# Performance work log

Hardware: AMD Instinct MI355X
Metric: run time of the kernel (lower is better)

## Reference

```python
import jax, jax.numpy as jnp
import numpy as np

N = 100000

def gat_layer(x, src, dst, W, a_s, a_d, b, H, C, concat):
    # x: [N, F_in]; messages flow src -> dst, softmax grouped by dst (PyG GATConv)
    h = (x @ W).reshape(N, H, C)                       # [N,H,C]
    al_s = jnp.sum(h * a_s, axis=-1)                   # [N,H]
    al_d = jnp.sum(h * a_d, axis=-1)                   # [N,H]
    e = jax.nn.leaky_relu(al_s[src] + al_d[dst], 0.2)  # [E,H]
    m = jax.ops.segment_max(e, dst, num_segments=N)    # [N,H] per-dst max
    ex = jnp.exp(e - m[dst])
    s = jax.ops.segment_sum(ex, dst, num_segments=N)
    alpha = ex / (s[dst] + 1e-16)                      # [E,H]
    msg = h[src] * alpha[:, :, None]                   # [E,H,C]
    out = jax.ops.segment_sum(msg, dst, num_segments=N)  # [N,H,C]
    out = out.reshape(N, H * C) if concat else out.mean(axis=1)
    return out + b

def setup_inputs() -> dict:
    key = jax.random.key(0)
    ks = jax.random.split(key, 32)
    d = {}
    d['x'] = jax.random.normal(ks[0], (N, 128), dtype=jnp.float32)
    d['edge_index'] = jax.random.randint(ks[1], (2, 1600000), 0, N, dtype=jnp.int32)
    dims = [(128, 8, 8), (64, 8, 8), (64, 8, 8), (64, 8, 8), (64, 8, 40)]
    for i, (fin, H, C) in enumerate(dims, start=1):
        d[f'W{i}'] = jax.random.normal(ks[4 * i], (fin, H * C), dtype=jnp.float32) * 0.1
        d[f'as{i}'] = jax.random.normal(ks[4 * i + 1], (H, C), dtype=jnp.float32) * 0.1
        d[f'ad{i}'] = jax.random.normal(ks[4 * i + 2], (H, C), dtype=jnp.float32) * 0.1
        d[f'b{i}'] = jnp.zeros((H * C if i < 5 else C,), dtype=jnp.float32)
    return d

def reference(x, edge_index, W1, as1, ad1, b1, W2, as2, ad2, b2, W3, as3, ad3, b3, W4, as4, ad4, b4, W5, as5, ad5, b5):
    # add self-loops (PyG GATConv default add_self_loops=True)
    loop = jnp.arange(N, dtype=edge_index.dtype)
    src = jnp.concatenate([edge_index[0], loop])
    dst = jnp.concatenate([edge_index[1], loop])
    h = gat_layer(x, src, dst, W1, as1, ad1, b1, 8, 8, True)
    h = jax.nn.leaky_relu(h, 0.2)  # dropout is identity in eval mode
    h = gat_layer(h, src, dst, W2, as2, ad2, b2, 8, 8, True)
    h = jax.nn.leaky_relu(h, 0.2)
    h = gat_layer(h, src, dst, W3, as3, ad3, b3, 8, 8, True)
    h = jax.nn.leaky_relu(h, 0.2)
    h = gat_layer(h, src, dst, W4, as4, ad4, b4, 8, 8, True)
    h = jax.nn.leaky_relu(h, 0.2)
    h = gat_layer(h, src, dst, W5, as5, ad5, b5, 8, 40, False)
    return jax.nn.log_softmax(h, axis=1)
```

## Files before the change

### kernel.cpp

```cpp
#include <hip/hip_runtime.h>
#include <cstddef>
#include <cstdint>

static __device__ __forceinline__ float leaky(float x){ return x >= 0.f ? x : 0.2f*x; }
static __device__ __forceinline__ float bfl(unsigned short v){ return __uint_as_float(((unsigned)v)<<16); }
static __device__ __forceinline__ float blo(unsigned u){ return __uint_as_float(u<<16); }
static __device__ __forceinline__ float bhi(unsigned u){ return __uint_as_float(u & 0xffff0000u); }
static __device__ __forceinline__ unsigned bf16r(float f){
  unsigned u = __float_as_uint(f);
  return (u + 0x7fffu + ((u>>16)&1u)) >> 16;
}
static __device__ __forceinline__ unsigned pk(float lo, float hi){
  return bf16r(lo) | (bf16r(hi)<<16);
}

__global__ __launch_bounds__(256) void rs_hist1(const int* __restrict__ edst, int E, int N,
                                                int* __restrict__ hist, int NBLK, int Etot){
  __shared__ int lh[512];
  int t = threadIdx.x, b = blockIdx.x;
  lh[t] = 0; lh[t+256] = 0;
  __syncthreads();
  int base = b*8192;
  for (int i = 0; i < 32; i++){
    int e = base + t + i*256;
    if (e < Etot){
      int d = (e < E) ? edst[e] : (e - E);
      atomicAdd(&lh[d>>8], 1);
    }
  }
  __syncthreads();
  hist[(size_t)t*NBLK + b] = lh[t];
  hist[(size_t)(t+256)*NBLK + b] = lh[t+256];
}
__global__ __launch_bounds__(256) void s_bsum(const int* __restrict__ a, int* __restrict__ bsum, int L){
  __shared__ int sm[256];
  int t = threadIdx.x; int i = blockIdx.x*256 + t;
  sm[t] = (i < L) ? a[i] : 0;
  __syncthreads();
  #pragma unroll
  for (int o=128;o;o>>=1){ if (t<o) sm[t]+=sm[t+o]; __syncthreads(); }
  if (t==0) bsum[blockIdx.x] = sm[0];
}
__global__ __launch_bounds__(512) void k_bscan(const int* __restrict__ bsum, int* __restrict__ boff, int NB){
  __shared__ int sm[512];
  int t = threadIdx.x;
  int v = (t < NB) ? bsum[t] : 0;
  sm[t] = v; __syncthreads();
  for (int o=1;o<512;o<<=1){
    int u = (t>=o) ? sm[t-o] : 0;
    __syncthreads();
    sm[t] += u;
    __syncthreads();
  }
  if (t < NB) boff[t] = sm[t] - v;
  if (t == NB-1) boff[NB] = sm[t];
}
__global__ __launch_bounds__(256) void s_apply(const int* __restrict__ a, const int* __restrict__ boff,
                                               int* __restrict__ out, int L){
  __shared__ int sm[256];
  int t = threadIdx.x, b = blockIdx.x;
  int i = b*256 + t;
  int v = (i < L) ? a[i] : 0;
  sm[t] = v; __syncthreads();
  for (int o=1;o<256;o<<=1){
    int u = (t>=o) ? sm[t-o] : 0;
    __syncthreads();
    sm[t] += u;
    __syncthreads();
  }
  if (i < L) out[i] = boff[b] + sm[t] - v;
}
__global__ __launch_bounds__(256) void rs_scatter1(const int* __restrict__ esrc, const int* __restrict__ edst,
                                                   int E, int N, const int* __restrict__ hist2, int NBLK,
                                                   int2* __restrict__ bufA, int Etot){
  __shared__ int gb[512];
  __shared__ int lcnt[512];
  int t = threadIdx.x, b = blockIdx.x;
  gb[t]     = hist2[(size_t)t*NBLK + b];
  gb[t+256] = hist2[(size_t)(t+256)*NBLK + b];
  lcnt[t] = 0; lcnt[t+256] = 0;
  __syncthreads();
  int base = b*8192;
  for (int i = 0; i < 32; i++){
    int e = base + t + i*256;
    if (e < Etot){
      int s, d;
      if (e < E){ s = esrc[e]; d = edst[e]; }
      else { s = e - E; d = s; }
      int bin = d >> 8;
      int r = atomicAdd(&lcnt[bin], 1);
      bufA[gb[bin] + r] = make_int2(s, d);
    }
  }
}
__global__ __launch_bounds__(256) void rs_lvl2(const int2* __restrict__ bufA, const int* __restrict__ hist2,
                                               int NBLK, int* __restrict__ srcs, int* __restrict__ off,
                                               int N, int Etot){
  __shared__ int cnt[256];
  __shared__ int basev[256];
  int t = threadIdx.x, g = blockIdx.x;
  int beg = hist2[(size_t)g*NBLK];
  int end = (g < 511) ? hist2[(size_t)(g+1)*NBLK] : Etot;
  cnt[t] = 0;
  __syncthreads();
  for (int j = beg + t; j < end; j += 256)
    atomicAdd(&cnt[bufA[j].y & 255], 1);
  __syncthreads();
  int v = cnt[t];
  for (int o=1;o<256;o<<=1){
    int u = (t>=o) ? cnt[t-o] : 0;
    __syncthreads();
    cnt[t] += u;
    __syncthreads();
  }
  basev[t] = cnt[t] - v;
  __syncthreads();
  cnt[t] = 0;
  __syncthreads();
  for (int j = beg + t; j < end; j += 256){
    int2 p = bufA[j];
    int lb = p.y & 255;
    int r = atomicAdd(&cnt[lb], 1);
    srcs[beg + basev[lb] + r] = p.x;
  }
  int node = g*256 + t;
  if (node < N) off[node] = beg + basev[t];
  if (g == 0 && t == 0) off[N] = Etot;
}

template<int K, int M, bool OB>
__global__ __launch_bounds__(256) void k_gemm(
    const float* __restrict__ A, const float* __restrict__ W, int ldw, int col0,
    void* __restrict__ out, int N)
{
  constexpr int KT = 64;
  constexpr int TX = M/4;
  __shared__ float As[64][KT+1];
  __shared__ alignas(16) float Ws[KT][M];
  int t = threadIdx.x;
  int base = blockIdx.x*64;
  int tx = t % TX, ty = t / TX;
  bool act = ty < 16;
  int n0 = ty*4, m0 = tx*4;
  float acc[4][4] = {};
  for (int kt=0; kt<K; kt+=KT){
    for (int i=t; i<64*(KT/4); i+=256){
      int n  = i >> 4;
      int kq = i & 15;
      float4 v = make_float4(0.f,0.f,0.f,0.f);
      int gn = base + n;
      if (gn < N) v = *(const float4*)(A + (size_t)gn*K + kt + kq*4);
      As[n][kq*4+0]=v.x; As[n][kq*4+1]=v.y; As[n][kq*4+2]=v.z; As[n][kq*4+3]=v.w;
    }
    for (int i=t; i<KT*(M/4); i+=256){
      int k = i/(M/4), mq = i%(M/4);
      *(float4*)&Ws[k][mq*4] = *(const float4*)(W + (size_t)(kt+k)*ldw + col0 + mq*4);
    }
    __syncthreads();
    if (act){
      #pragma unroll 8
      for (int k=0;k<KT;k++){
        float4 w = *(const float4*)&Ws[k][m0];
        float av0 = As[n0+0][k], av1 = As[n0+1][k], av2 = As[n0+2][k], av3 = As[n0+3][k];
        acc[0][0]=fmaf(av0,w.x,acc[0][0]); acc[0][1]=fmaf(av0,w.y,acc[0][1]);
        acc[0][2]=fmaf(av0,w.z,acc[0][2]); acc[0][3]=fmaf(av0,w.w,acc[0][3]);
        acc[1][0]=fmaf(av1,w.x,acc[1][0]); acc[1][1]=fmaf(av1,w.y,acc[1][1]);
        acc[1][2]=fmaf(av1,w.z,acc[1][2]); acc[1][3]=fmaf(av1,w.w,acc[1][3]);
        acc[2][0]=fmaf(av2,w.x,acc[2][0]); acc[2][1]=fmaf(av2,w.y,acc[2][1]);
        acc[2][2]=fmaf(av2,w.z,acc[2][2]); acc[2][3]=fmaf(av2,w.w,acc[2][3]);
        acc[3][0]=fmaf(av3,w.x,acc[3][0]); acc[3][1]=fmaf(av3,w.y,acc[3][1]);
        acc[3][2]=fmaf(av3,w.z,acc[3][2]); acc[3][3]=fmaf(av3,w.w,acc[3][3]);
      }
    }
    __syncthreads();
  }
  if (act){
    #pragma unroll
    for (int i=0;i<4;i++){
      int gn = base + n0 + i;
      if (gn < N){
        if (OB){
          unsigned p0 = pk(acc[i][0], acc[i][1]);
          unsigned p1 = pk(acc[i][2], acc[i][3]);
          *(uint2*)((unsigned short*)out + (size_t)gn*M + m0) = make_uint2(p0, p1);
        } else {
          float4 v = make_float4(acc[i][0],acc[i][1],acc[i][2],acc[i][3]);
          *(float4*)((float*)out + (size_t)gn*M + m0) = v;
        }
      }
    }
  }
}

__global__ __launch_bounds__(320) void k_gemm5(
    const unsigned short* __restrict__ z16, const float* __restrict__ Wf,
    float* __restrict__ out5, int base, int cnt)
{
  __shared__ float As[64][65];
  __shared__ alignas(16) float Ws[64][40];
  int t = threadIdx.x;
  int rb = blockIdx.x*64;
  int tx = t % 10, ty = t / 10;
  int n0 = ty*2, m0 = tx*4;
  float acc[2][4] = {};
  for (int kt = 0; kt < 512; kt += 64){
    for (int i = t; i < 512; i += 320){
      int n = i >> 3, kq = i & 7;
      uint4 q = make_uint4(0,0,0,0);
      int ln = rb + n;
      if (ln < cnt) q = *(const uint4*)(z16 + (size_t)ln*512 + kt + kq*8);
      float* ap = &As[n][kq*8];
      ap[0]=blo(q.x); ap[1]=bhi(q.x); ap[2]=blo(q.y); ap[3]=bhi(q.y);
      ap[4]=blo(q.z); ap[5]=bhi(q.z); ap[6]=blo(q.w); ap[7]=bhi(q.w);
    }
    for (int i = t; i < 640; i += 320){
      int k = i / 10, mq = i % 10;
      *(float4*)&Ws[k][mq*4] = *(const float4*)(Wf + (size_t)(kt+k)*40 + mq*4);
    }
    __syncthreads();
    #pragma unroll 8
    for (int k=0;k<64;k++){
      float4 w = *(const float4*)&Ws[k][m0];
      float a0 = As[n0][k], a1 = As[n0+1][k];
      acc[0][0]=fmaf(a0,w.x,acc[0][0]); acc[0][1]=fmaf(a0,w.y,acc[0][1]);
      acc[0][2]=fmaf(a0,w.z,acc[0][2]); acc[0][3]=fmaf(a0,w.w,acc[0][3]);
      acc[1][0]=fmaf(a1,w.x,acc[1][0]); acc[1][1]=fmaf(a1,w.y,acc[1][1]);
      acc[1][2]=fmaf(a1,w.z,acc[1][2]); acc[1][3]=fmaf(a1,w.w,acc[1][3]);
    }
    __syncthreads();
  }
  #pragma unroll
  for (int r=0;r<2;r++){
    int ln = rb + n0 + r;
    if (ln < cnt){
      *(float4*)(out5 + (size_t)(base+ln)*40 + m0) =
        make_float4(acc[r][0],acc[r][1],acc[r][2],acc[r][3]);
    }
  }
}

__global__ void k_al(const unsigned short* __restrict__ h16, const float* __restrict__ a_s,
                     const float* __restrict__ a_d, unsigned short* __restrict__ al_s16,
                     float* __restrict__ al_d, int total )
{
  int idx = blockIdx.x*256 + threadIdx.x;
  if (idx >= total) return;
  int hd = idx & 7;
  uint4 q = *(const uint4*)(h16 + (size_t)idx*8);
  const float4* sp = (const float4*)(a_s + hd*8);
  const float4* dp = (const float4*)(a_d + hd*8);
  float4 s0 = sp[0], s1 = sp[1], d0 = dp[0], d1 = dp[1];
  float f0=blo(q.x), f1=bhi(q.x), f2=blo(q.y), f3=bhi(q.y);
  float f4=blo(q.z), f5=bhi(q.z), f6=blo(q.w), f7=bhi(q.w);
  float s = f0*s0.x + f1*s0.y + f2*s0.z + f3*s0.w
          + f4*s1.x + f5*s1.y + f6*s1.z + f7*s1.w;
  float d = f0*d0.x + f1*d0.y + f2*d0.z + f3*d0.w
          + f4*d1.x + f5*d1.y + f6*d1.z + f7*d1.w;
  al_s16[idx] = (unsigned short)bf16r(s);
  al_d[idx] = d;
}

template<bool OB>
__global__ __launch_bounds__(256) void k_agg64(
    const unsigned short* __restrict__ h16, const unsigned short* __restrict__ al16,
    const float* __restrict__ al_d, const int* __restrict__ off,
    const int* __restrict__ srcs, const float* __restrict__ bias,
    void* __restrict__ outf, int N, int apply_act)
{
  int t = threadIdx.x;
  int grp = t >> 3;
  int sub = t & 7;
  int node = blockIdx.x*32 + grp;
  if (node >= N) return;
  int beg = off[node], end = off[node+1];
  float ald = al_d[(size_t)node*8 + sub];
  float s = 0.f;
  float acc[8] = {0.f,0.f,0.f,0.f,0.f,0.f,0.f,0.f};
  int j = beg;
  for (; j+3 < end; j += 4){
    int s0 = srcs[j], s1 = srcs[j+1], s2 = srcs[j+2], s3 = srcs[j+3];
    float e0 = leaky(bfl(al16[(size_t)s0*8 + sub]) + ald);
    float e1 = leaky(bfl(al16[(size_t)s1*8 + sub]) + ald);
    float e2 = leaky(bfl(al16[(size_t)s2*8 + sub]) + ald);
    float e3 = leaky(bfl(al16[(size_t)s3*8 + sub]) + ald);
    float a0 = __expf(e0), a1 = __expf(e1), a2 = __expf(e2), a3 = __expf(e3);
    uint4 q0 = *(const uint4*)(h16 + (size_t)s0*64 + sub*8);
    uint4 q1 = *(const uint4*)(h16 + (size_t)s1*64 + sub*8);
    uint4 q2 = *(const uint4*)(h16 + (size_t)s2*64 + sub*8);
    uint4 q3 = *(const uint4*)(h16 + (size_t)s3*64 + sub*8);
    s += a0 + a1 + a2 + a3;
    acc[0]=fmaf(a0,blo(q0.x),acc[0]); acc[1]=fmaf(a0,bhi(q0.x),acc[1]);
    acc[2]=fmaf(a0,blo(q0.y),acc[2]); acc[3]=fmaf(a0,bhi(q0.y),acc[3]);
    acc[4]=fmaf(a0,blo(q0.z),acc[4]); acc[5]=fmaf(a0,bhi(q0.z),acc[5]);
    acc[6]=fmaf(a0,blo(q0.w),acc[6]); acc[7]=fmaf(a0,bhi(q0.w),acc[7]);
    acc[0]=fmaf(a1,blo(q1.x),acc[0]); acc[1]=fmaf(a1,bhi(q1.x),acc[1]);
    acc[2]=fmaf(a1,blo(q1.y),acc[2]); acc[3]=fmaf(a1,bhi(q1.y),acc[3]);
    acc[4]=fmaf(a1,blo(q1.z),acc[4]); acc[5]=fmaf(a1,bhi(q1.z),acc[5]);
    acc[6]=fmaf(a1,blo(q1.w),acc[6]); acc[7]=fmaf(a1,bhi(q1.w),acc[7]);
    acc[0]=fmaf(a2,blo(q2.x),acc[0]); acc[1]=fmaf(a2,bhi(q2.x),acc[1]);
    acc[2]=fmaf(a2,blo(q2.y),acc[2]); acc[3]=fmaf(a2,bhi(q2.y),acc[3]);
    acc[4]=fmaf(a2,blo(q2.z),acc[4]); acc[5]=fmaf(a2,bhi(q2.z),acc[5]);
    acc[6]=fmaf(a2,blo(q2.w),acc[6]); acc[7]=fmaf(a2,bhi(q2.w),acc[7]);
    acc[0]=fmaf(a3,blo(q3.x),acc[0]); acc[1]=fmaf(a3,bhi(q3.x),acc[1]);
    acc[2]=fmaf(a3,blo(q3.y),acc[2]); acc[3]=fmaf(a3,bhi(q3.y),acc[3]);
    acc[4]=fmaf(a3,blo(q3.z),acc[4]); acc[5]=fmaf(a3,bhi(q3.z),acc[5]);
    acc[6]=fmaf(a3,blo(q3.w),acc[6]); acc[7]=fmaf(a3,bhi(q3.w),acc[7]);
  }
  for (; j < end; ++j){
    int s0 = srcs[j];
    float e0 = leaky(bfl(al16[(size_t)s0*8 + sub]) + ald);
    float a0 = __expf(e0);
    uint4 q0 = *(const uint4*)(h16 + (size_t)s0*64 + sub*8);
    s += a0;
    acc[0]=fmaf(a0,blo(q0.x),acc[0]); acc[1]=fmaf(a0,bhi(q0.x),acc[1]);
    acc[2]=fmaf(a0,blo(q0.y),acc[2]); acc[3]=fmaf(a0,bhi(q0.y),acc[3]);
    acc[4]=fmaf(a0,blo(q0.z),acc[4]); acc[5]=fmaf(a0,bhi(q0.z),acc[5]);
    acc[6]=fmaf(a0,blo(q0.w),acc[6]); acc[7]=fmaf(a0,bhi(q0.w),acc[7]);
  }
  float inv = 1.f/(s + 1e-16f);
  const float4* bp = (const float4*)(bias + sub*8);
  float4 b0 = bp[0], b1 = bp[1];
  float r0 = acc[0]*inv + b0.x, r1 = acc[1]*inv + b0.y;
  float r2 = acc[2]*inv + b0.z, r3 = acc[3]*inv + b0.w;
  float r4 = acc[4]*inv + b1.x, r5 = acc[5]*inv + b1.y;
  float r6 = acc[6]*inv + b1.z, r7 = acc[7]*inv + b1.w;
  if (apply_act){
    r0=leaky(r0); r1=leaky(r1); r2=leaky(r2); r3=leaky(r3);
    r4=leaky(r4); r5=leaky(r5); r6=leaky(r6); r7=leaky(r7);
  }
  if (OB){
    uint4 o;
    o.x = pk(r0,r1); o.y = pk(r2,r3); o.z = pk(r4,r5); o.w = pk(r6,r7);
    *(uint4*)((unsigned short*)outf + (size_t)node*64 + sub*8) = o;
  } else {
    float* op = (float*)outf + (size_t)node*64 + sub*8;
    *(float4*)op = make_float4(r0,r1,r2,r3);
    *(float4*)(op+4) = make_float4(r4,r5,r6,r7);
  }
}

__global__ __launch_bounds__(512) void k_ws(const float* __restrict__ W5,
                                            const float* __restrict__ as5,
                                            const float* __restrict__ ad5,
                                            float* __restrict__ ws, float* __restrict__ wd){
  int t = threadIdx.x;
  int h = t >> 6, k = t & 63;
  float s = 0.f, d = 0.f;
  #pragma unroll 8
  for (int c=0;c<40;c++){
    float w = W5[(size_t)k*320 + h*40 + c];
    s = fmaf(w, as5[h*40+c], s);
    d = fmaf(w, ad5[h*40+c], d);
  }
  ws[h*64+k] = s; wd[h*64+k] = d;
}
__global__ void k_wf(const float* __restrict__ W5, float* __restrict__ Wf){
  int i = blockIdx.x*256 + threadIdx.x;
  if (i >= 512*40) return;
  int row = i / 40, c = i - row*40;
  int h = row >> 6, k = row & 63;
  Wf[i] = W5[(size_t)k*320 + h*40 + c];
}
__global__ void k_al5b(const unsigned short* __restrict__ f16, const float* __restrict__ ws,
                       const float* __restrict__ wd, unsigned short* __restrict__ al_s16,
                       float* __restrict__ al_d, int total )
{
  int idx = blockIdx.x*256 + threadIdx.x;
  if (idx >= total) return;
  int n = idx >> 3, h = idx & 7;
  const uint4* fp = (const uint4*)(f16 + (size_t)n*64);
  const float4* ap = (const float4*)(ws + h*64);
  const float4* bp = (const float4*)(wd + h*64);
  float s = 0.f, d = 0.f;
  #pragma unroll
  for (int q=0;q<8;q++){
    uint4 f = fp[q];
    float4 a0 = ap[q*2], a1 = ap[q*2+1];
    float4 b0 = bp[q*2], b1 = bp[q*2+1];
    float f0=blo(f.x), f1=bhi(f.x), f2=blo(f.y), f3=bhi(f.y);
    float f4=blo(f.z), f5=bhi(f.z), f6=blo(f.w), f7=bhi(f.w);
    s += f0*a0.x + f1*a0.y + f2*a0.z + f3*a0.w + f4*a1.x + f5*a1.y + f6*a1.z + f7*a1.w;
    d += f0*b0.x + f1*b0.y + f2*b0.z + f3*b0.w + f4*b1.x + f5*b1.y + f6*b1.z + f7*b1.w;
  }
  al_s16[idx] = (unsigned short)bf16r(s);
  al_d[idx] = d;
}

__global__ __launch_bounds__(256) void k_agg5z(
    const unsigned short* __restrict__ f16, const unsigned short* __restrict__ al16,
    const float* __restrict__ al_d, const int* __restrict__ off,
    const int* __restrict__ srcs, unsigned short* __restrict__ z16, int base, int cnt)
{
  int t = threadIdx.x;
  int w = t >> 6;
  int ln = blockIdx.x*4 + w;
  if (ln >= cnt) return;
  int node = base + ln;
  int tl = t & 63;
  int hd = tl & 7;
  int cb = tl >> 3;
  int beg = off[node], end = off[node+1];
  float ald = al_d[(size_t)node*8 + hd];
  int lanebase = hd*4;
  int cbo = cb*8;
  float s = 0.f;
  float acc[8] = {0.f,0.f,0.f,0.f,0.f,0.f,0.f,0.f};
  for (int jb = beg; jb < end; jb += 8){
    int j = jb + cb;
    float atil = 0.f; int si = 0;
    if (j < end){
      si = srcs[j];
      atil = __expf(leaky(bfl(al16[(size_t)si*8 + hd]) + ald));
    }
    s += atil;
    #pragma unroll 8
    for (int e = 0; e < 8; e++){
      if (jb + e >= end) break;
      float ae = __uint_as_float(__builtin_amdgcn_ds_bpermute(lanebase + e*32, __float_as_uint(atil)));
      int sie = __builtin_amdgcn_readlane(si, e*8);
      uint4 q = *(const uint4*)(f16 + (size_t)sie*64 + cbo);
      acc[0]=fmaf(ae,blo(q.x),acc[0]); acc[1]=fmaf(ae,bhi(q.x),acc[1]);
      acc[2]=fmaf(ae,blo(q.y),acc[2]); acc[3]=fmaf(ae,bhi(q.y),acc[3]);
      acc[4]=fmaf(ae,blo(q.z),acc[4]); acc[5]=fmaf(ae,bhi(q.z),acc[5]);
      acc[6]=fmaf(ae,blo(q.w),acc[6]); acc[7]=fmaf(ae,bhi(q.w),acc[7]);
    }
  }
  s += __shfl_xor(s, 8, 64);
  s += __shfl_xor(s, 16, 64);
  s += __shfl_xor(s, 32, 64);
  float inv = 1.f/(s + 1e-16f);
  uint4 o;
  o.x = pk(acc[0]*inv, acc[1]*inv);
  o.y = pk(acc[2]*inv, acc[3]*inv);
  o.z = pk(acc[4]*inv, acc[5]*inv);
  o.w = pk(acc[6]*inv, acc[7]*inv);
  *(uint4*)(z16 + (size_t)ln*512 + hd*64 + cbo) = o;
}

__global__ __launch_bounds__(256) void k_final(
    const float* __restrict__ acc, const float* __restrict__ b5,
    float* __restrict__ out, int N)
{
  int t = threadIdx.x;
  int node = blockIdx.x*4 + (t >> 6);
  if (node >= N) return;
  int tl = t & 63;
  float v = (tl < 40) ? acc[(size_t)node*40 + tl]*0.125f + b5[tl] : -1e30f;
  float m = v;
  #pragma unroll
  for (int o=32;o;o>>=1) m = fmaxf(m, __shfl_xor(m, o, 64));
  float ex = (tl < 40) ? __expf(v - m) : 0.f;
  float s = ex;
  #pragma unroll
  for (int o=32;o;o>>=1) s += __shfl_xor(s, o, 64);
  if (tl < 40) out[(size_t)node*40 + tl] = (v - m) - __logf(s);
}

extern "C" void kernel_launch(void* const* d_in, const int* in_sizes, int n_in,
                              void* d_out, int out_size, void* d_ws, size_t ws_size,
                              hipStream_t stream) {
  const float* x  = (const float*)d_in[0];
  const int*   ei = (const int*)d_in[1];
  const int N = in_sizes[0] / 128;
  const int E = in_sizes[1] / 2;
  const int* esrc = ei;
  const int* edst = ei + E;
  const float* W1 = (const float*)d_in[2];
  const float* as1= (const float*)d_in[3];
  const float* ad1= (const float*)d_in[4];
  const float* b1 = (const float*)d_in[5];
  const float* W2 = (const float*)d_in[6];
  const float* as2= (const float*)d_in[7];
  const float* ad2= (const float*)d_in[8];
  const float* b2 = (const float*)d_in[9];
  const float* W3 = (const float*)d_in[10];
  const float* as3= (const float*)d_in[11];
  const float* ad3= (const float*)d_in[12];
  const float* b3 = (const float*)d_in[13];
  const float* W4 = (const float*)d_in[14];
  const float* as4= (const float*)d_in[15];
  const float* ad4= (const float*)d_in[16];
  const float* b4 = (const float*)d_in[17];
  const float* W5 = (const float*)d_in[18];
  const float* as5= (const float*)d_in[19];
  const float* ad5= (const float*)d_in[20];
  const float* b5 = (const float*)d_in[21];

  char* p = (char*)d_ws;
  auto alloc = [&](size_t bytes)->void*{
    uintptr_t u = (uintptr_t)p;
    u = (u + 255) & ~(uintptr_t)255;
    void* r = (void*)u;
    p = (char*)u + bytes;
    return r;
  };
  const int Etot = E + N;
  const int NBLK = (Etot + 8191)/8192;
  const int L    = 512*NBLK;
  const int NB2  = (L + 255)/256;
  const int NG   = (N + 255)/256;

  int* off    = (int*)alloc((size_t)(N+1)*4);
  int* srcs   = (int*)alloc((size_t)Etot*4);
  int* hist   = (int*)alloc((size_t)L*4);
  int* hist2  = (int*)alloc((size_t)L*4);
  int* hb     = (int*)alloc((size_t)(NB2+1)*4);
  unsigned short* al_s16 = (unsigned short*)alloc((size_t)N*8*2);
  float* al_d = (float*)alloc((size_t)N*8*4);
  unsigned short* h16  = (unsigned short*)alloc((size_t)N*64*2);
  unsigned short* fB16 = (unsigned short*)alloc((size_t)N*64*2);
  float* featA= (float*)alloc((size_t)N*64*4);
  float* featB= (float*)alloc((size_t)N*64*4);
  float* wsb  = (float*)alloc((size_t)8*64*4);
  float* wdb  = (float*)alloc((size_t)8*64*4);
  float* Wf   = (float*)alloc((size_t)512*40*4);
  float* out5 = (float*)alloc((size_t)N*40*4);
  unsigned short* zbuf = (unsigned short*)featA;
  int2* bufA  = (int2*)featA;

  int gT = (N+63)/64, gA = (N+3)/4;
  int gA64 = (N+31)/32;
  int gAl = (N*8+255)/256;

  rs_hist1  <<<NBLK,256,0,stream>>>(edst, E, N, hist, NBLK, Etot);
  s_bsum    <<<NB2,256,0,stream>>>(hist, hb, L);
  k_bscan   <<<1,512,0,stream>>>(hb, hb, NB2);
  s_apply   <<<NB2,256,0,stream>>>(hist, hb, hist2, L);
  rs_scatter1<<<NBLK,256,0,stream>>>(esrc, edst, E, N, hist2, NBLK, bufA, Etot);
  rs_lvl2   <<<NG,256,0,stream>>>(bufA, hist2, NBLK, srcs, off, N, Etot);

  k_gemm<128,64,true><<<gT,256,0,stream>>>(x, W1, 64, 0, h16, N);
  k_al<<<gAl,256,0,stream>>>(h16, as1, ad1, al_s16, al_d, N*8);
  k_agg64<false><<<gA64,256,0,stream>>>(h16, al_s16, al_d, off, srcs, b1, featA, N, 1);

  k_gemm<64,64,true><<<gT,256,0,stream>>>(featA, W2, 64, 0, h16, N);
  k_al<<<gAl,256,0,stream>>>(h16, as2, ad2, al_s16, al_d, N*8);
  k_agg64<false><<<gA64,256,0,stream>>>(h16, al_s16, al_d, off, srcs, b2, featB, N, 1);

  k_gemm<64,64,true><<<gT,256,0,stream>>>(featB, W3, 64, 0, h16, N);
  k_al<<<gAl,256,0,stream>>>(h16, as3, ad3, al_s16, al_d, N*8);
  k_agg64<false><<<gA64,256,0,stream>>>(h16, al_s16, al_d, off, srcs, b3, featA, N, 1);

  k_gemm<64,64,true><<<gT,256,0,stream>>>(featA, W4, 64, 0, h16, N);
  k_al<<<gAl,256,0,stream>>>(h16, as4, ad4, al_s16, al_d, N*8);
  k_agg64<true><<<gA64,256,0,stream>>>(h16, al_s16, al_d, off, srcs, b4, fB16, N, 1);

  k_ws  <<<1,512,0,stream>>>(W5, as5, ad5, wsb, wdb);
  k_wf  <<<(512*40+255)/256,256,0,stream>>>(W5, Wf);
  k_al5b<<<gAl,256,0,stream>>>(fB16, wsb, wdb, al_s16, al_d, N*8);
  const int CH = 50000;
  for (int base = 0; base < N; base += CH){
    int cnt = (N - base < CH) ? (N - base) : CH;
    k_agg5z<<<(cnt+3)/4,256,0,stream>>>(fB16, al_s16, al_d, off, srcs, zbuf, base, cnt);
    k_gemm5<<<(cnt+63)/64,320,0,stream>>>(zbuf, Wf, out5, base, cnt);
  }

  k_final<<<gA,256,0,stream>>>(out5, b5, (float*)d_out, N);
}
```

Baseline: 653.3 us.

## Use bf16 hidden features, recompute source attention in aggregation, pack sort buffer

Intermediate layer features are now stored as bf16 and read by a GEMM that takes a bf16-input template path, halving activation traffic between layers. The 64-wide aggregation now assigns a wavefront per node, with 8 edge slots per head. It recomputes the source attention logit from the gathered h row instead of gathering a separate al_s array, then reduces across slots with shuffles. The radix sort's intermediate buffer packs source id (17 bits) and low dst bits into one int. Layer-5 aggregation gets a one-step software prefetch of the next edge batch, and the chunk size is halved so zbuf can alias h16 and fA16. Risks are the extra per-edge dot-product ALU work and the wider shuffle reduction, plus the 17-bit packing, which assumes N stays below 131072.

```diff
diff --git a/kernel.cpp b/kernel.cpp
--- a/kernel.cpp
+++ b/kernel.cpp
@@ -72,7 +72,7 @@
 }
 __global__ __launch_bounds__(256) void rs_scatter1(const int* __restrict__ esrc, const int* __restrict__ edst,
                                                    int E, int N, const int* __restrict__ hist2, int NBLK,
-                                                   int2* __restrict__ bufA, int Etot){
+                                                   int* __restrict__ bufA, int Etot){
   __shared__ int gb[512];
   __shared__ int lcnt[512];
   int t = threadIdx.x, b = blockIdx.x;
@@ -89,11 +89,11 @@
       else { s = e - E; d = s; }
       int bin = d >> 8;
       int r = atomicAdd(&lcnt[bin], 1);
-      bufA[gb[bin] + r] = make_int2(s, d);
-    }
-  }
-}
-__global__ __launch_bounds__(256) void rs_lvl2(const int2* __restrict__ bufA, const int* __restrict__ hist2,
+      bufA[gb[bin] + r] = s | ((d & 255) << 17);
+    }
+  }
+}
+__global__ __launch_bounds__(256) void rs_lvl2(const int* __restrict__ bufA, const int* __restrict__ hist2,
                                                int NBLK, int* __restrict__ srcs, int* __restrict__ off,
                                                int N, int Etot){
   __shared__ int cnt[256];
@@ -104,7 +104,7 @@
   cnt[t] = 0;
   __syncthreads();
   for (int j = beg + t; j < end; j += 256)
-    atomicAdd(&cnt[bufA[j].y & 255], 1);
+    atomicAdd(&cnt[(bufA[j] >> 17) & 255], 1);
   __syncthreads();
   int v = cnt[t];
   for (int o=1;o<256;o<<=1){
@@ -118,19 +118,19 @@
   cnt[t] = 0;
   __syncthreads();
   for (int j = beg + t; j < end; j += 256){
-    int2 p = bufA[j];
-    int lb = p.y & 255;
+    int u = bufA[j];
+    int lb = (u >> 17) & 255;
     int r = atomicAdd(&cnt[lb], 1);
-    srcs[beg + basev[lb] + r] = p.x;
+    srcs[beg + basev[lb] + r] = u & 0x1FFFF;
   }
   int node = g*256 + t;
   if (node < N) off[node] = beg + basev[t];
   if (g == 0 && t == 0) off[N] = Etot;
 }
 
-template<int K, int M, bool OB>
+template<int K, int M, bool IB, bool OB>
 __global__ __launch_bounds__(256) void k_gemm(
-    const float* __restrict__ A, const float* __restrict__ W, int ldw, int col0,
+    const void* __restrict__ Ain, const float* __restrict__ W, int ldw, int col0,
     void* __restrict__ out, int N)
 {
   constexpr int KT = 64;
@@ -144,13 +144,27 @@
   int n0 = ty*4, m0 = tx*4;
   float acc[4][4] = {};
   for (int kt=0; kt<K; kt+=KT){
-    for (int i=t; i<64*(KT/4); i+=256){
-      int n  = i >> 4;
-      int kq = i & 15;
-      float4 v = make_float4(0.f,0.f,0.f,0.f);
-      int gn = base + n;
-      if (gn < N) v = *(const float4*)(A + (size_t)gn*K + kt + kq*4);
-      As[n][kq*4+0]=v.x; As[n][kq*4+1]=v.y; As[n][kq*4+2]=v.z; As[n][kq*4+3]=v.w;
+    if (IB){
+      const unsigned short* A16 = (const unsigned short*)Ain;
+      for (int i=t; i<64*8; i+=256){
+        int n = i >> 3, kq = i & 7;
+        uint4 q = make_uint4(0,0,0,0);
+        int gn = base + n;
+        if (gn < N) q = *(const uint4*)(A16 + (size_t)gn*K + kt + kq*8);
+        float* ap = &As[n][kq*8];
+        ap[0]=blo(q.x); ap[1]=bhi(q.x); ap[2]=blo(q.y); ap[3]=bhi(q.y);
+        ap[4]=blo(q.z); ap[5]=bhi(q.z); ap[6]=blo(q.w); ap[7]=bhi(q.w);
+      }
+    } else {
+      const float* A = (const float*)Ain;
+      for (int i=t; i<64*16; i+=256){
+        int n  = i >> 4;
+        int kq = i & 15;
+        float4 v = make_float4(0.f,0.f,0.f,0.f);
+        int gn = base + n;
+        if (gn < N) v = *(const float4*)(A + (size_t)gn*K + kt + kq*4);
+        As[n][kq*4+0]=v.x; As[n][kq*4+1]=v.y; As[n][kq*4+2]=v.z; As[n][kq*4+3]=v.w;
+      }
     }
     for (int i=t; i<KT*(M/4); i+=256){
       int k = i/(M/4), mq = i%(M/4);
@@ -239,86 +253,72 @@
   }
 }
 
-__global__ void k_al(const unsigned short* __restrict__ h16, const float* __restrict__ a_s,
-                     const float* __restrict__ a_d, unsigned short* __restrict__ al_s16,
+__global__ void k_al(const unsigned short* __restrict__ h16, const float* __restrict__ a_d,
                      float* __restrict__ al_d, int total )
 {
   int idx = blockIdx.x*256 + threadIdx.x;
   if (idx >= total) return;
   int hd = idx & 7;
   uint4 q = *(const uint4*)(h16 + (size_t)idx*8);
-  const float4* sp = (const float4*)(a_s + hd*8);
   const float4* dp = (const float4*)(a_d + hd*8);
-  float4 s0 = sp[0], s1 = sp[1], d0 = dp[0], d1 = dp[1];
+  float4 d0 = dp[0], d1 = dp[1];
   float f0=blo(q.x), f1=bhi(q.x), f2=blo(q.y), f3=bhi(q.y);
   float f4=blo(q.z), f5=bhi(q.z), f6=blo(q.w), f7=bhi(q.w);
-  float s = f0*s0.x + f1*s0.y + f2*s0.z + f3*s0.w
-          + f4*s1.x + f5*s1.y + f6*s1.z + f7*s1.w;
-  float d = f0*d0.x + f1*d0.y + f2*d0.z + f3*d0.w
-          + f4*d1.x + f5*d1.y + f6*d1.z + f7*d1.w;
-  al_s16[idx] = (unsigned short)bf16r(s);
-  al_d[idx] = d;
-}
-
-template<bool OB>
+  al_d[idx] = f0*d0.x + f1*d0.y + f2*d0.z + f3*d0.w
+            + f4*d1.x + f5*d1.y + f6*d1.z + f7*d1.w;
+}
+
 __global__ __launch_bounds__(256) void k_agg64(
-    const unsigned short* __restrict__ h16, const unsigned short* __restrict__ al16,
+    const unsigned short* __restrict__ h16, const float* __restrict__ a_s,
     const float* __restrict__ al_d, const int* __restrict__ off,
     const int* __restrict__ srcs, const float* __restrict__ bias,
-    void* __restrict__ outf, int N, int apply_act)
-{
-  int t = threadIdx.x;
-  int grp = t >> 3;
-  int sub = t & 7;
-  int node = blockIdx.x*32 + grp;
+    unsigned short* __restrict__ outf, int N, int apply_act)
+{
+  int t = threadIdx.x;
+  int node = blockIdx.x*4 + (t >> 6);
   if (node >= N) return;
+  int tl = t & 63;
+  int hd = tl >> 3;
+  int slot = tl & 7;
   int beg = off[node], end = off[node+1];
-  float ald = al_d[(size_t)node*8 + sub];
+  float ald = al_d[(size_t)node*8 + hd];
+  const float4* asp = (const float4*)(a_s + hd*8);
+  float4 as0 = asp[0], as1 = asp[1];
   float s = 0.f;
   float acc[8] = {0.f,0.f,0.f,0.f,0.f,0.f,0.f,0.f};
-  int j = beg;
-  for (; j+3 < end; j += 4){
-    int s0 = srcs[j], s1 = srcs[j+1], s2 = srcs[j+2], s3 = srcs[j+3];
-    float e0 = leaky(bfl(al16[(size_t)s0*8 + sub]) + ald);
-    float e1 = leaky(bfl(al16[(size_t)s1*8 + sub]) + ald);
-    float e2 = leaky(bfl(al16[(size_t)s2*8 + sub]) + ald);
-    float e3 = leaky(bfl(al16[(size_t)s3*8 + sub]) + ald);
-    float a0 = __expf(e0), a1 = __expf(e1), a2 = __expf(e2), a3 = __expf(e3);
-    uint4 q0 = *(const uint4*)(h16 + (size_t)s0*64 + sub*8);
-    uint4 q1 = *(const uint4*)(h16 + (size_t)s1*64 + sub*8);
-    uint4 q2 = *(const uint4*)(h16 + (size_t)s2*64 + sub*8);
-    uint4 q3 = *(const uint4*)(h16 + (size_t)s3*64 + sub*8);
-    s += a0 + a1 + a2 + a3;
-    acc[0]=fmaf(a0,blo(q0.x),acc[0]); acc[1]=fmaf(a0,bhi(q0.x),acc[1]);
-    acc[2]=fmaf(a0,blo(q0.y),acc[2]); acc[3]=fmaf(a0,bhi(q0.y),acc[3]);
-    acc[4]=fmaf(a0,blo(q0.z),acc[4]); acc[5]=fmaf(a0,bhi(q0.z),acc[5]);
-    acc[6]=fmaf(a0,blo(q0.w),acc[6]); acc[7]=fmaf(a0,bhi(q0.w),acc[7]);
-    acc[0]=fmaf(a1,blo(q1.x),acc[0]); acc[1]=fmaf(a1,bhi(q1.x),acc[1]);
-    acc[2]=fmaf(a1,blo(q1.y),acc[2]); acc[3]=fmaf(a1,bhi(q1.y),acc[3]);
-    acc[4]=fmaf(a1,blo(q1.z),acc[4]); acc[5]=fmaf(a1,bhi(q1.z),acc[5]);
-    acc[6]=fmaf(a1,blo(q1.w),acc[6]); acc[7]=fmaf(a1,bhi(q1.w),acc[7]);
-    acc[0]=fmaf(a2,blo(q2.x),acc[0]); acc[1]=fmaf(a2,bhi(q2.x),acc[1]);
-    acc[2]=fmaf(a2,blo(q2.y),acc[2]); acc[3]=fmaf(a2,bhi(q2.y),acc[3]);
-    acc[4]=fmaf(a2,blo(q2.z),acc[4]); acc[5]=fmaf(a2,bhi(q2.z),acc[5]);
-    acc[6]=fmaf(a2,blo(q2.w),acc[6]); acc[7]=fmaf(a2,bhi(q2.w),acc[7]);
-    acc[0]=fmaf(a3,blo(q3.x),acc[0]); acc[1]=fmaf(a3,bhi(q3.x),acc[1]);
-    acc[2]=fmaf(a3,blo(q3.y),acc[2]); acc[3]=fmaf(a3,bhi(q3.y),acc[3]);
-    acc[4]=fmaf(a3,blo(q3.z),acc[4]); acc[5]=fmaf(a3,bhi(q3.z),acc[5]);
-    acc[6]=fmaf(a3,blo(q3.w),acc[6]); acc[7]=fmaf(a3,bhi(q3.w),acc[7]);
-  }
-  for (; j < end; ++j){
-    int s0 = srcs[j];
-    float e0 = leaky(bfl(al16[(size_t)s0*8 + sub]) + ald);
-    float a0 = __expf(e0);
-    uint4 q0 = *(const uint4*)(h16 + (size_t)s0*64 + sub*8);
-    s += a0;
-    acc[0]=fmaf(a0,blo(q0.x),acc[0]); acc[1]=fmaf(a0,bhi(q0.x),acc[1]);
-    acc[2]=fmaf(a0,blo(q0.y),acc[2]); acc[3]=fmaf(a0,bhi(q0.y),acc[3]);
-    acc[4]=fmaf(a0,blo(q0.z),acc[4]); acc[5]=fmaf(a0,bhi(q0.z),acc[5]);
-    acc[6]=fmaf(a0,blo(q0.w),acc[6]); acc[7]=fmaf(a0,bhi(q0.w),acc[7]);
+  for (int jb = beg; jb < end; jb += 16){
+    int j0 = jb + slot, j1 = jb + 8 + slot;
+    uint4 q0 = make_uint4(0,0,0,0), q1 = make_uint4(0,0,0,0);
+    if (j0 < end){ int s0 = srcs[j0]; q0 = *(const uint4*)(h16 + (size_t)s0*64 + hd*8); }
+    if (j1 < end){ int s1 = srcs[j1]; q1 = *(const uint4*)(h16 + (size_t)s1*64 + hd*8); }
+    float f00=blo(q0.x), f01=bhi(q0.x), f02=blo(q0.y), f03=bhi(q0.y);
+    float f04=blo(q0.z), f05=bhi(q0.z), f06=blo(q0.w), f07=bhi(q0.w);
+    float f10=blo(q1.x), f11=bhi(q1.x), f12=blo(q1.y), f13=bhi(q1.y);
+    float f14=blo(q1.z), f15=bhi(q1.z), f16=blo(q1.w), f17=bhi(q1.w);
+    float e0 = f00*as0.x + f01*as0.y + f02*as0.z + f03*as0.w
+             + f04*as1.x + f05*as1.y + f06*as1.z + f07*as1.w + ald;
+    float e1 = f10*as0.x + f11*as0.y + f12*as0.z + f13*as0.w
+             + f14*as1.x + f15*as1.y + f16*as1.z + f17*as1.w + ald;
+    float a0 = (j0 < end) ? __expf(leaky(e0)) : 0.f;
+    float a1 = (j1 < end) ? __expf(leaky(e1)) : 0.f;
+    s += a0 + a1;
+    acc[0]=fmaf(a0,f00,acc[0]); acc[1]=fmaf(a0,f01,acc[1]);
+    acc[2]=fmaf(a0,f02,acc[2]); acc[3]=fmaf(a0,f03,acc[3]);
+    acc[4]=fmaf(a0,f04,acc[4]); acc[5]=fmaf(a0,f05,acc[5]);
+    acc[6]=fmaf(a0,f06,acc[6]); acc[7]=fmaf(a0,f07,acc[7]);
+    acc[0]=fmaf(a1,f10,acc[0]); acc[1]=fmaf(a1,f11,acc[1]);
+    acc[2]=fmaf(a1,f12,acc[2]); acc[3]=fmaf(a1,f13,acc[3]);
+    acc[4]=fmaf(a1,f14,acc[4]); acc[5]=fmaf(a1,f15,acc[5]);
+    acc[6]=fmaf(a1,f16,acc[6]); acc[7]=fmaf(a1,f17,acc[7]);
+  }
+  #pragma unroll
+  for (int m=1;m<8;m<<=1){
+    s += __shfl_xor(s, m, 64);
+    #pragma unroll
+    for (int i=0;i<8;i++) acc[i] += __shfl_xor(acc[i], m, 64);
   }
   float inv = 1.f/(s + 1e-16f);
-  const float4* bp = (const float4*)(bias + sub*8);
+  const float4* bp = (const float4*)(bias + hd*8);
   float4 b0 = bp[0], b1 = bp[1];
   float r0 = acc[0]*inv + b0.x, r1 = acc[1]*inv + b0.y;
   float r2 = acc[2]*inv + b0.z, r3 = acc[3]*inv + b0.w;
@@ -328,14 +328,10 @@
     r0=leaky(r0); r1=leaky(r1); r2=leaky(r2); r3=leaky(r3);
     r4=leaky(r4); r5=leaky(r5); r6=leaky(r6); r7=leaky(r7);
   }
-  if (OB){
+  if (slot == 0){
     uint4 o;
     o.x = pk(r0,r1); o.y = pk(r2,r3); o.z = pk(r4,r5); o.w = pk(r6,r7);
-    *(uint4*)((unsigned short*)outf + (size_t)node*64 + sub*8) = o;
-  } else {
-    float* op = (float*)outf + (size_t)node*64 + sub*8;
-    *(float4*)op = make_float4(r0,r1,r2,r3);
-    *(float4*)(op+4) = make_float4(r4,r5,r6,r7);
+    *(uint4*)(outf + (size_t)node*64 + hd*8) = o;
   }
 }
 
@@ -405,17 +401,24 @@
   int cbo = cb*8;
   float s = 0.f;
   float acc[8] = {0.f,0.f,0.f,0.f,0.f,0.f,0.f,0.f};
-  for (int jb = beg; jb < end; jb += 8){
+  int jb = beg;
+  float atil = 0.f; int si = 0;
+  {
     int j = jb + cb;
-    float atil = 0.f; int si = 0;
-    if (j < end){
-      si = srcs[j];
-      atil = __expf(leaky(bfl(al16[(size_t)si*8 + hd]) + ald));
+    if (j < end){ si = srcs[j]; atil = __expf(leaky(bfl(al16[(size_t)si*8 + hd]) + ald)); }
+  }
+  while (jb < end){
+    int jb2 = jb + 8;
+    float atil2 = 0.f; int si2 = 0;
+    {
+      int j2 = jb2 + cb;
+      if (j2 < end){ si2 = srcs[j2]; atil2 = __expf(leaky(bfl(al16[(size_t)si2*8 + hd]) + ald)); }
     }
     s += atil;
+    int nfull = end - jb; if (nfull > 8) nfull = 8;
     #pragma unroll 8
     for (int e = 0; e < 8; e++){
-      if (jb + e >= end) break;
+      if (e >= nfull) break;
       float ae = __uint_as_float(__builtin_amdgcn_ds_bpermute(lanebase + e*32, __float_as_uint(atil)));
       int sie = __builtin_amdgcn_readlane(si, e*8);
       uint4 q = *(const uint4*)(f16 + (size_t)sie*64 + cbo);
@@ -424,6 +427,7 @@
       acc[4]=fmaf(ae,blo(q.z),acc[4]); acc[5]=fmaf(ae,bhi(q.z),acc[5]);
       acc[6]=fmaf(ae,blo(q.w),acc[6]); acc[7]=fmaf(ae,bhi(q.w),acc[7]);
     }
+    atil = atil2; si = si2; jb = jb2;
   }
   s += __shfl_xor(s, 8, 64);
   s += __shfl_xor(s, 16, 64);
@@ -508,18 +512,16 @@
   unsigned short* al_s16 = (unsigned short*)alloc((size_t)N*8*2);
   float* al_d = (float*)alloc((size_t)N*8*4);
   unsigned short* h16  = (unsigned short*)alloc((size_t)N*64*2);
+  unsigned short* fA16 = (unsigned short*)alloc((size_t)N*64*2);
   unsigned short* fB16 = (unsigned short*)alloc((size_t)N*64*2);
-  float* featA= (float*)alloc((size_t)N*64*4);
-  float* featB= (float*)alloc((size_t)N*64*4);
   float* wsb  = (float*)alloc((size_t)8*64*4);
   float* wdb  = (float*)alloc((size_t)8*64*4);
   float* Wf   = (float*)alloc((size_t)512*40*4);
   float* out5 = (float*)alloc((size_t)N*40*4);
-  unsigned short* zbuf = (unsigned short*)featA;
-  int2* bufA  = (int2*)featA;
+  unsigned short* zbuf = h16;
+  int* bufA   = (int*)h16;
 
   int gT = (N+63)/64, gA = (N+3)/4;
-  int gA64 = (N+31)/32;
   int gAl = (N*8+255)/256;
 
   rs_hist1  <<<NBLK,256,0,stream>>>(edst, E, N, hist, NBLK, Etot);
@@ -529,26 +531,26 @@
   rs_scatter1<<<NBLK,256,0,stream>>>(esrc, edst, E, N, hist2, NBLK, bufA, Etot);
   rs_lvl2   <<<NG,256,0,stream>>>(bufA, hist2, NBLK, srcs, off, N, Etot);
 
-  k_gemm<128,64,true><<<gT,256,0,stream>>>(x, W1, 64, 0, h16, N);
-  k_al<<<gAl,256,0,stream>>>(h16, as1, ad1, al_s16, al_d, N*8);
-  k_agg64<false><<<gA64,256,0,stream>>>(h16, al_s16, al_d, off, srcs, b1, featA, N, 1);
-
-  k_gemm<64,64,true><<<gT,256,0,stream>>>(featA, W2, 64, 0, h16, N);
-  k_al<<<gAl,256,0,stream>>>(h16, as2, ad2, al_s16, al_d, N*8);
-  k_agg64<false><<<gA64,256,0,stream>>>(h16, al_s16, al_d, off, srcs, b2, featB, N, 1);
-
-  k_gemm<64,64,true><<<gT,256,0,stream>>>(featB, W3, 64, 0, h16, N);
-  k_al<<<gAl,256,0,stream>>>(h16, as3, ad3, al_s16, al_d, N*8);
-  k_agg64<false><<<gA64,256,0,stream>>>(h16, al_s16, al_d, off, srcs, b3, featA, N, 1);
-
-  k_gemm<64,64,true><<<gT,256,0,stream>>>(featA, W4, 64, 0, h16, N);
-  k_al<<<gAl,256,0,stream>>>(h16, as4, ad4, al_s16, al_d, N*8);
-  k_agg64<true><<<gA64,256,0,stream>>>(h16, al_s16, al_d, off, srcs, b4, fB16, N, 1);
+  k_gemm<128,64,false,true><<<gT,256,0,stream>>>(x, W1, 64, 0, h16, N);
+  k_al<<<gAl,256,0,stream>>>(h16, ad1, al_d, N*8);
+  k_agg64<<<gA,256,0,stream>>>(h16, as1, al_d, off, srcs, b1, fA16, N, 1);
+
+  k_gemm<64,64,true,true><<<gT,256,0,stream>>>(fA16, W2, 64, 0, h16, N);
+  k_al<<<gAl,256,0,stream>>>(h16, ad2, al_d, N*8);
+  k_agg64<<<gA,256,0,stream>>>(h16, as2, al_d, off, srcs, b2, fB16, N, 1);
+
+  k_gemm<64,64,true,true><<<gT,256,0,stream>>>(fB16, W3, 64, 0, h16, N);
+  k_al<<<gAl,256,0,stream>>>(h16, ad3, al_d, N*8);
+  k_agg64<<<gA,256,0,stream>>>(h16, as3, al_d, off, srcs, b3, fA16, N, 1);
+
+  k_gemm<64,64,true,true><<<gT,256,0,stream>>>(fA16, W4, 64, 0, h16, N);
+  k_al<<<gAl,256,0,stream>>>(h16, ad4, al_d, N*8);
+  k_agg64<<<gA,256,0,stream>>>(h16, as4, al_d, off, srcs, b4, fB16, N, 1);
 
   k_ws  <<<1,512,0,stream>>>(W5, as5, ad5, wsb, wdb);
   k_wf  <<<(512*40+255)/256,256,0,stream>>>(W5, Wf);
   k_al5b<<<gAl,256,0,stream>>>(fB16, wsb, wdb, al_s16, al_d, N*8);
-  const int CH = 50000;
+  const int CH = 25000;
   for (int base = 0; base < N; base += CH){
     int cnt = (N - base < CH) ? (N - base) : CH;
     k_agg5z<<<(cnt+3)/4,256,0,stream>>>(fB16, al_s16, al_d, off, srcs, zbuf, base, cnt);
```

Result: slower. 761.2 us (+16.5%).
